# Kernel optimization log

Measured on AMD Instinct MI355X. Metric: run time of the kernel, lower is better.

The kernel has to match this reference:

```python
import jax, jax.numpy as jnp
import numpy as np

N = 8192  # number of proposals


def setup_inputs() -> dict:
    key = jax.random.key(0)
    k1, k2, k3 = jax.random.split(key, 3)
    xy = jax.random.uniform(k1, (N, 2), dtype=jnp.float32) * 1000.0   # top-left corners
    wh = jax.random.uniform(k2, (N, 2), dtype=jnp.float32) * 120.0 + 4.0  # widths/heights
    conf = jax.random.uniform(k3, (N, 1), dtype=jnp.float32)
    preds = jnp.concatenate([xy, xy + wh, conf], axis=1)  # [N,5] x1,y1,x2,y2,conf
    return {"preds": preds, "thresh": 0.5, "max_proposals": 1000}


def _nms_keep_mask(boxes_sorted, thresh):
    # boxes_sorted: [N,4] sorted by descending confidence
    x1, y1, x2, y2 = (boxes_sorted[:, i] for i in range(4))
    area = (x2 - x1) * (y2 - y1)                               # [N]
    ix1 = jnp.maximum(x1[:, None], x1[None, :])
    iy1 = jnp.maximum(y1[:, None], y1[None, :])
    ix2 = jnp.minimum(x2[:, None], x2[None, :])
    iy2 = jnp.minimum(y2[:, None], y2[None, :])
    iw = jnp.maximum(ix2 - ix1, 0.0)
    ih = jnp.maximum(iy2 - iy1, 0.0)
    inter = iw * ih                                            # [N,N]
    iou = inter / (area[:, None] + area[None, :] - inter + 1e-12)
    n = boxes_sorted.shape[0]
    later = jnp.arange(n)[None, :] > jnp.arange(n)[:, None]    # strictly lower-priority boxes

    def body(i, keep):
        # if box i survives, suppress all later boxes overlapping it above thresh
        sup = keep[i] & later[i] & (iou[i] > thresh)
        return keep & ~sup

    return jax.lax.fori_loop(0, n, body, jnp.ones((n,), dtype=bool))


def reference(preds, thresh, max_proposals):
    # thresh < 0 -> identity (original early return); implemented with thresh >= 0 path
    order = jnp.argsort(-preds[:, 4])          # descending confidence
    boxes_sorted = preds[order, :4]
    keep = _nms_keep_mask(boxes_sorted, thresh)  # [N] bool, in sorted order
    n = preds.shape[0]
    # stable pack: kept positions first (ascending = descending confidence), pad at end
    rank = jnp.where(keep, jnp.arange(n), n)
    pos = jnp.argsort(rank)[:max_proposals]     # [M] positions in sorted order
    valid = keep[pos]                           # [M] which slots are real
    keep_idx = jnp.where(valid, order[pos], -1)  # indices into original preds, -1 pad
    kept = preds[jnp.clip(keep_idx, 0)]          # [M,5]
    kept = jnp.where(valid[:, None], kept, 0.0)
    return kept, keep_idx
```

## Files before the change

### kernel.cpp

```cpp
#include <hip/hip_runtime.h>

typedef unsigned long long u64;

#define FSLOTS 16
#define RCUT 2048

__device__ __forceinline__ u64 bcast64(u64 v, int b) {
  unsigned lo = __builtin_amdgcn_readlane((unsigned)v, b);
  unsigned hi = __builtin_amdgcn_readlane((unsigned)(v >> 32), b);
  return ((u64)hi << 32) | lo;
}
__device__ __forceinline__ u64 sgpr64(u64 v) {
  unsigned lo = __builtin_amdgcn_readfirstlane((unsigned)v);
  unsigned hi = __builtin_amdgcn_readfirstlane((unsigned)(v >> 32));
  return ((u64)hi << 32) | lo;
}
__device__ __forceinline__ u64 wor64(u64 v) {
#pragma unroll
  for (int off = 32; off; off >>= 1) v |= __shfl_xor(v, off, 64);
  return v;
}

#define APPLYJ(JV, T)                                                      \
  if ((T) < lim_) {                                                        \
    int j_ = (JV);                                                         \
    atomicAnd(&live[j_ >> 6], ~((u64)1 << (j_ & 63)));                     \
  }

#define CHUNK(c, BND, RC, LA, LB, LC, LD)                                  \
  if (out < maxp && (c) < nch) {                                           \
    u64 rem_ = sgpr64(live[(c)]);                                          \
    if (rem_) {                                                            \
      u64 K_;                                                              \
      u64 my_ = ((rem_ >> lane) & 1) ? (BND) : 0;                          \
      u64 A_ = sgpr64(wor64(my_));                                         \
      u64 hot_ = rem_ & A_;                                                \
      if (!hot_) {                                                         \
        K_ = rem_;                                                         \
      } else {                                                             \
        u64 defK_ = rem_ & ~A_;                                            \
        u64 myk_ = ((defK_ >> lane) & 1) ? (BND) : 0;                      \
        u64 S_ = sgpr64(wor64(myk_));                                      \
        K_ = defK_;                                                        \
        while (hot_) {                                                     \
          int b_ = __builtin_amdgcn_readfirstlane(                         \
              (int)__builtin_ctzll(hot_));                                 \
          hot_ &= hot_ - 1;                                                \
          if (!((S_ >> b_) & 1)) {                                         \
            K_ |= (u64)1 << b_;                                            \
            S_ |= bcast64(BND, b_);                                        \
          }                                                                \
        }                                                                  \
      }                                                                    \
      int kc_ = (int)__popcll(K_);                                         \
      bool mine_ = (K_ >> lane) & 1;                                       \
      if (mine_) {                                                         \
        int pos_ = out + (int)__popcll(K_ & (((u64)1 << lane) - 1));       \
        if (pos_ < maxp) sel[pos_] = (c) * 64 + lane;                      \
      }                                                                    \
      out += kc_;                                                          \
      if (kc_ > 0 && out < maxp) {                                         \
        int lim_ = mine_ ? ((RC) < FSLOTS ? (RC) : FSLOTS) : 0;            \
        APPLYJ((LA).x, 0)  APPLYJ((LA).y, 1)                               \
        APPLYJ((LA).z, 2)  APPLYJ((LA).w, 3)                               \
        APPLYJ((LB).x, 4)  APPLYJ((LB).y, 5)                               \
        APPLYJ((LB).z, 6)  APPLYJ((LB).w, 7)                               \
        APPLYJ((LC).x, 8)  APPLYJ((LC).y, 9)                               \
        APPLYJ((LC).z, 10) APPLYJ((LC).w, 11)                              \
        APPLYJ((LD).x, 12) APPLYJ((LD).y, 13)                              \
        APPLYJ((LD).z, 14) APPLYJ((LD).w, 15)                              \
        u64 ovf_ = __ballot(mine_ && (RC) > FSLOTS);                       \
        while (ovf_) {                                                     \
          int l_ = (int)__builtin_ctzll(ovf_);                             \
          ovf_ &= ovf_ - 1;                                                \
          int r_ = (c) * 64 + l_;                                          \
          u64 v0_ = (2 * lane < nch)                                       \
                        ? M[(size_t)r_ * nw + 2 * lane] : 0ULL;            \
          u64 v1_ = (2 * lane + 1 < nch)                                   \
                        ? M[(size_t)r_ * nw + 2 * lane + 1] : 0ULL;        \
          live[2 * lane] &= ~v0_;                                          \
          live[2 * lane + 1] &= ~v1_;                                      \
        }                                                                  \
      }                                                                    \
    }                                                                      \
    {                                                                      \
      int cc_ = (c) + 4;                                                   \
      if (cc_ < nch) {                                                     \
        int r_ = cc_ * 64 + lane;                                          \
        int rr_ = r_ < n ? r_ : n - 1;                                     \
        BND = D1[rr_];                                                     \
        RC = rowcnt[rr_];                                                  \
        const int4* lp_ = (const int4*)(rowlist + (size_t)rr_ * FSLOTS);   \
        LA = lp_[0]; LB = lp_[1]; LC = lp_[2]; LD = lp_[3];                \
      }                                                                    \
    }                                                                      \
  }

#define PREF(cc, BND, RC, LA, LB, LC, LD)                                  \
  if ((cc) < nch) {                                                        \
    int r_ = (cc) * 64 + lane;                                             \
    int rr_ = r_ < n ? r_ : n - 1;                                         \
    BND = D1[rr_];                                                         \
    RC = rowcnt[rr_];                                                      \
    const int4* lp_ = (const int4*)(rowlist + (size_t)rr_ * FSLOTS);       \
    LA = lp_[0]; LB = lp_[1]; LC = lp_[2]; LD = lp_[3];                    \
  }

#define SCAN_BODY(NCH_)                                                    \
  int nch = (NCH_);                                                        \
  for (int w = lane; w < 128; w += 64) {                                   \
    u64 m = 0;                                                             \
    if (w < nw) {                                                          \
      long long hi = (long long)(w + 1) * 64;                              \
      m = (hi <= n) ? ~0ULL                                                \
                    : ((n > (long long)w * 64)                             \
                           ? (((u64)1 << (n - w * 64)) - 1) : 0ULL);       \
    }                                                                      \
    live[w] = m;                                                           \
  }                                                                        \
  u64 b0 = 0, b1 = 0, b2 = 0, b3 = 0;                                      \
  int rc0 = 0, rc1 = 0, rc2 = 0, rc3 = 0;                                  \
  int4 l00 = {0,0,0,0}, l01 = {0,0,0,0}, l02 = {0,0,0,0}, l03 = {0,0,0,0}; \
  int4 l10 = {0,0,0,0}, l11 = {0,0,0,0}, l12 = {0,0,0,0}, l13 = {0,0,0,0}; \
  int4 l20 = {0,0,0,0}, l21 = {0,0,0,0}, l22 = {0,0,0,0}, l23 = {0,0,0,0}; \
  int4 l30 = {0,0,0,0}, l31 = {0,0,0,0}, l32 = {0,0,0,0}, l33 = {0,0,0,0}; \
  PREF(0, b0, rc0, l00, l01, l02, l03)                                     \
  PREF(1, b1, rc1, l10, l11, l12, l13)                                     \
  PREF(2, b2, rc2, l20, l21, l22, l23)                                     \
  PREF(3, b3, rc3, l30, l31, l32, l33)                                     \
  int out = 0;                                                             \
  for (int kk = 0; kk < nch && out < maxp; kk += 4) {                      \
    CHUNK(kk + 0, b0, rc0, l00, l01, l02, l03)                             \
    CHUNK(kk + 1, b1, rc1, l10, l11, l12, l13)                             \
    CHUNK(kk + 2, b2, rc2, l20, l21, l22, l23)                             \
    CHUNK(kk + 3, b3, rc3, l30, l31, l32, l33)                             \
  }

__device__ __forceinline__ void do_tile(int wx, int ry, int lane,
                                        const float4* sb4, float4* cb,
                                        float* cbar, int n, float th,
                                        u64* M, u64* D1, int* rowcnt,
                                        int* rowlist, int nw) {
  int col0 = wx * 64;
  int cj = col0 + lane;
  int cjc = cj < n ? cj : n - 1;
  {
    float4 b4 = sb4[cjc];
    cb[lane] = b4;
    cbar[lane] = __fmul_rn(__fsub_rn(b4.z, b4.x), __fsub_rn(b4.w, b4.y));
  }
  int row = ry * 64 + lane;
  if (row >= n) return;
  float4 r4 = sb4[row];
  float rarea = __fmul_rn(__fsub_rn(r4.z, r4.x), __fsub_rn(r4.w, r4.y));
  u64 w = 0;
#pragma unroll 8
  for (int j = 0; j < 64; ++j) {
    float4 c4 = cb[j];
    float ix1 = fmaxf(r4.x, c4.x);
    float iy1 = fmaxf(r4.y, c4.y);
    float ix2 = fminf(r4.z, c4.z);
    float iy2 = fminf(r4.w, c4.w);
    float iw = fmaxf(__fsub_rn(ix2, ix1), 0.0f);
    float ih = fmaxf(__fsub_rn(iy2, iy1), 0.0f);
    float inter = __fmul_rn(iw, ih);
    float denom = __fadd_rn(__fsub_rn(__fadd_rn(rarea, cbar[j]), inter), 1e-12f);
    float iou = __fdiv_rn(inter, denom);
    int col = col0 + j;
    bool sup = (col > row) && (col < n) && (iou > th);
    w |= ((u64)sup) << j;
  }
  M[(size_t)row * nw + wx] = w;
  if (wx == ry) D1[row] = w;
  int pcw = (int)__popcll(w);
  if (pcw) {
    int base = atomicAdd(&rowcnt[row], pcw);
    u64 w2 = w;
    int k = 0;
    while (w2) {
      int j = (int)__builtin_ctzll(w2);
      w2 &= w2 - 1;
      int idx = base + k;
      if (idx < FSLOTS) rowlist[(size_t)row * FSLOTS + idx] = col0 + j;
      ++k;
    }
  }
}

__device__ __forceinline__ void tri_decode(int u, int* wxo, int* ryo) {
  int w = (int)((sqrtf(8.0f * u + 1.0f) - 1.0f) * 0.5f);
  while ((w + 1) * (w + 2) / 2 <= u) ++w;
  while (w * (w + 1) / 2 > u) --w;
  *wxo = w;
  *ryo = u - w * (w + 1) / 2;
}

__global__ __launch_bounds__(256)
void k_rank(const float* __restrict__ preds, int n,
            float* __restrict__ sboxes, int* __restrict__ sidx,
            int* __restrict__ rowcnt) {
  __shared__ float cs[8192];
  int t = threadIdx.x;
  int b = blockIdx.x;
  for (int j = t; j < n; j += 256) cs[j] = preds[j * 5 + 4];
  {
    int zi = b * 32 + t;
    if (t < 32 && zi < n) rowcnt[zi] = 0;
  }
  __syncthreads();

  int row = b * 32 + (t >> 3);
  int sub = t & 7;
  int cw = (((n + 7) >> 3) + 3) & ~3;
  int cnt = 0;
  if (row < n) {
    float ci = cs[row];
    int start = sub * cw;
    int end = start + cw; if (end > n) end = n;
    const float4* cs4 = (const float4*)cs;
    int s4 = start >> 2, e4 = end >> 2;
    for (int j4 = s4; j4 < e4; ++j4) {
      float4 c4 = cs4[j4];
      int jb = j4 * 4;
      cnt += (c4.x > ci) || (c4.x == ci && (jb + 0) < row);
      cnt += (c4.y > ci) || (c4.y == ci && (jb + 1) < row);
      cnt += (c4.z > ci) || (c4.z == ci && (jb + 2) < row);
      cnt += (c4.w > ci) || (c4.w == ci && (jb + 3) < row);
    }
    for (int j = e4 * 4; j < end; ++j)
      cnt += (cs[j] > ci) || (cs[j] == ci && j < row);
  }
  cnt += __shfl_down(cnt, 4, 8);
  cnt += __shfl_down(cnt, 2, 8);
  cnt += __shfl_down(cnt, 1, 8);
  if (sub == 0 && row < n) {
    int pos = cnt;
    sboxes[pos * 4 + 0] = preds[row * 5 + 0];
    sboxes[pos * 4 + 1] = preds[row * 5 + 1];
    sboxes[pos * 4 + 2] = preds[row * 5 + 2];
    sboxes[pos * 4 + 3] = preds[row * 5 + 3];
    sidx[pos] = row;
  }
}

__global__ __launch_bounds__(64)
void k_mask_lo(const float* __restrict__ sboxes, int n,
               const float* __restrict__ thr_p,
               u64* __restrict__ M, u64* __restrict__ D1,
               int* __restrict__ rowcnt, int* __restrict__ rowlist, int nw) {
  __shared__ float4 cb[64];
  __shared__ float cbar[64];
  int wx, ry;
  tri_decode(blockIdx.x, &wx, &ry);
  do_tile(wx, ry, threadIdx.x, (const float4*)sboxes, cb, cbar, n, *thr_p,
          M, D1, rowcnt, rowlist, nw);
}

__global__ __launch_bounds__(256, 1)
void k_finish(u64* __restrict__ M, u64* __restrict__ D1,
              int* __restrict__ rowcnt, int* __restrict__ rowlist,
              const float* __restrict__ preds, const float* __restrict__ thr_p,
              const float* __restrict__ sboxes, const int* __restrict__ sidx,
              int n, int nw, int maxp, int Rw,
              int* __restrict__ sel, float* __restrict__ outp) {
  __shared__ u64 live[128];
  __shared__ float4 cbw[4][64];
  __shared__ float cbarw[4][64];
  __shared__ int nk_s, done_s;
  int t = threadIdx.x;
  int wid = t >> 6;

  if (t < 64) {
    int lane = t;
    SCAN_BODY(Rw)
    if (lane == 0) {
      nk_s = (out < maxp) ? out : maxp;
      done_s = (out >= maxp || Rw >= nw) ? 1 : 0;
    }
  }
  __syncthreads();

  if (!done_s) {
    int loTri = (Rw * (Rw + 1)) / 2;
    int totTri = (nw * (nw + 1)) / 2;
    float th = *thr_p;
    const float4* sb4 = (const float4*)sboxes;
    for (int u = loTri + wid; u < totTri; u += 4) {
      int wx, ry;
      tri_decode(u, &wx, &ry);
      do_tile(wx, ry, t & 63, sb4, cbw[wid], cbarw[wid], n, th,
              M, D1, rowcnt, rowlist, nw);
    }
    __threadfence();
    __syncthreads();
    if (t < 64) {
      int lane = t;
      SCAN_BODY(nw)
      if (lane == 0) nk_s = (out < maxp) ? out : maxp;
    }
    __syncthreads();
  }

  int nk = nk_s;
  for (int k = t; k < maxp; k += 256) {
    if (k < nk) {
      int p = sel[k];
      int orig = sidx[p];
#pragma unroll
      for (int q = 0; q < 5; ++q) outp[k * 5 + q] = preds[orig * 5 + q];
      outp[(size_t)maxp * 5 + k] = (float)orig;
    } else {
#pragma unroll
      for (int q = 0; q < 5; ++q) outp[k * 5 + q] = 0.0f;
      outp[(size_t)maxp * 5 + k] = -1.0f;
    }
  }
}

extern "C" void kernel_launch(void* const* d_in, const int* in_sizes, int n_in,
                              void* d_out, int out_size, void* d_ws, size_t ws_size,
                              hipStream_t stream) {
  const float* preds = (const float*)d_in[0];
  const float* thr   = (const float*)d_in[1];
  float* out = (float*)d_out;
  int n    = in_sizes[0] / 5;
  int maxp = out_size / 6;
  int nw   = (n + 63) / 64;
  int Rw   = (RCUT / 64 < nw) ? RCUT / 64 : nw;
  int loTri = (Rw * (Rw + 1)) / 2;

  char* ws = (char*)d_ws;
  u64* M = (u64*)ws;
  size_t off = (size_t)n * nw * sizeof(u64);
  u64* D1 = (u64*)(ws + off);  off += (size_t)n * sizeof(u64);
  float* sboxes = (float*)(ws + off);  off += (size_t)n * 4 * sizeof(float);
  int*   sidx   = (int*)(ws + off);    off += (size_t)n * sizeof(int);
  int*   sel    = (int*)(ws + off);    off += (size_t)maxp * sizeof(int);
  int*   rowcnt = (int*)(ws + off);    off += (size_t)n * sizeof(int);
  int*   rowlist= (int*)(ws + off);

  hipLaunchKernelGGL(k_rank, dim3((n + 31) / 32), dim3(256), 0, stream,
                     preds, n, sboxes, sidx, rowcnt);
  hipLaunchKernelGGL(k_mask_lo, dim3(loTri), dim3(64), 0, stream,
                     sboxes, n, thr, M, D1, rowcnt, rowlist, nw);
  hipLaunchKernelGGL(k_finish, dim3(1), dim3(256), 0, stream,
                     M, D1, rowcnt, rowlist, preds, thr, sboxes, sidx,
                     n, nw, maxp, Rw, sel, out);
}
```

Measured before the change: 68.15 us.

## Fuse low-triangle mask kernel into finish kernel with flag-based grid barrier

Merges the triangle-tile mask kernel and the single-block finish kernel into one 256-block launch. Each block computes its share of tiles and publishes a release flag, and block 0 spin-waits on all flags before running the scan and tail work. This removes one kernel launch and its inter-kernel gap. The cost is the spin-wait, and correctness depends on all 256 blocks being co-resident (flags are reset in the prep kernel), with 4-wave blocks instead of single-wave ones.

```diff
diff --git a/kernel.cpp b/kernel.cpp
--- a/kernel.cpp
+++ b/kernel.cpp
@@ -4,6 +4,7 @@
 
 #define FSLOTS 16
 #define RCUT 2048
+#define NBLK 256
 
 __device__ __forceinline__ u64 bcast64(u64 v, int b) {
   unsigned lo = __builtin_amdgcn_readlane((unsigned)v, b);
@@ -196,9 +197,9 @@
 }
 
 __global__ __launch_bounds__(256)
-void k_rank(const float* __restrict__ preds, int n,
+void k_prep(const float* __restrict__ preds, int n,
             float* __restrict__ sboxes, int* __restrict__ sidx,
-            int* __restrict__ rowcnt) {
+            int* __restrict__ rowcnt, int* __restrict__ flags) {
   __shared__ float cs[8192];
   int t = threadIdx.x;
   int b = blockIdx.x;
@@ -206,6 +207,7 @@
   {
     int zi = b * 32 + t;
     if (t < 32 && zi < n) rowcnt[zi] = 0;
+    if (t == 0) flags[b] = 0;
   }
   __syncthreads();
 
@@ -243,32 +245,44 @@
   }
 }
 
-__global__ __launch_bounds__(64)
-void k_mask_lo(const float* __restrict__ sboxes, int n,
-               const float* __restrict__ thr_p,
-               u64* __restrict__ M, u64* __restrict__ D1,
-               int* __restrict__ rowcnt, int* __restrict__ rowlist, int nw) {
-  __shared__ float4 cb[64];
-  __shared__ float cbar[64];
-  int wx, ry;
-  tri_decode(blockIdx.x, &wx, &ry);
-  do_tile(wx, ry, threadIdx.x, (const float4*)sboxes, cb, cbar, n, *thr_p,
-          M, D1, rowcnt, rowlist, nw);
-}
-
 __global__ __launch_bounds__(256, 1)
-void k_finish(u64* __restrict__ M, u64* __restrict__ D1,
-              int* __restrict__ rowcnt, int* __restrict__ rowlist,
-              const float* __restrict__ preds, const float* __restrict__ thr_p,
-              const float* __restrict__ sboxes, const int* __restrict__ sidx,
-              int n, int nw, int maxp, int Rw,
-              int* __restrict__ sel, float* __restrict__ outp) {
+void k_main(u64* __restrict__ M, u64* __restrict__ D1,
+            int* __restrict__ rowcnt, int* __restrict__ rowlist,
+            const float* __restrict__ preds, const float* __restrict__ thr_p,
+            const float* __restrict__ sboxes, const int* __restrict__ sidx,
+            int n, int nw, int maxp, int Rw,
+            int* __restrict__ sel, int* __restrict__ flags,
+            float* __restrict__ outp) {
   __shared__ u64 live[128];
   __shared__ float4 cbw[4][64];
   __shared__ float cbarw[4][64];
   __shared__ int nk_s, done_s;
   int t = threadIdx.x;
+  int bid = blockIdx.x;
   int wid = t >> 6;
+  float th = *thr_p;
+  const float4* sb4 = (const float4*)sboxes;
+
+  {
+    int loTri = (Rw * (Rw + 1)) / 2;
+    for (int u = bid * 4 + wid; u < loTri; u += NBLK * 4) {
+      int wx, ry;
+      tri_decode(u, &wx, &ry);
+      do_tile(wx, ry, t & 63, sb4, cbw[wid], cbarw[wid], n, th,
+              M, D1, rowcnt, rowlist, nw);
+    }
+  }
+  __syncthreads();
+  if (t == 0) {
+    __threadfence();
+    __hip_atomic_store(&flags[bid], 1, __ATOMIC_RELEASE,
+                       __HIP_MEMORY_SCOPE_AGENT);
+  }
+  if (bid != 0) return;
+
+  while (__hip_atomic_load(&flags[t], __ATOMIC_ACQUIRE,
+                           __HIP_MEMORY_SCOPE_AGENT) == 0) {}
+  __syncthreads();
 
   if (t < 64) {
     int lane = t;
@@ -283,8 +297,6 @@
   if (!done_s) {
     int loTri = (Rw * (Rw + 1)) / 2;
     int totTri = (nw * (nw + 1)) / 2;
-    float th = *thr_p;
-    const float4* sb4 = (const float4*)sboxes;
     for (int u = loTri + wid; u < totTri; u += 4) {
       int wx, ry;
       tri_decode(u, &wx, &ry);
@@ -327,7 +339,6 @@
   int maxp = out_size / 6;
   int nw   = (n + 63) / 64;
   int Rw   = (RCUT / 64 < nw) ? RCUT / 64 : nw;
-  int loTri = (Rw * (Rw + 1)) / 2;
 
   char* ws = (char*)d_ws;
   u64* M = (u64*)ws;
@@ -337,13 +348,12 @@
   int*   sidx   = (int*)(ws + off);    off += (size_t)n * sizeof(int);
   int*   sel    = (int*)(ws + off);    off += (size_t)maxp * sizeof(int);
   int*   rowcnt = (int*)(ws + off);    off += (size_t)n * sizeof(int);
-  int*   rowlist= (int*)(ws + off);
-
-  hipLaunchKernelGGL(k_rank, dim3((n + 31) / 32), dim3(256), 0, stream,
-                     preds, n, sboxes, sidx, rowcnt);
-  hipLaunchKernelGGL(k_mask_lo, dim3(loTri), dim3(64), 0, stream,
-                     sboxes, n, thr, M, D1, rowcnt, rowlist, nw);
-  hipLaunchKernelGGL(k_finish, dim3(1), dim3(256), 0, stream,
+  int*   rowlist= (int*)(ws + off);    off += (size_t)n * FSLOTS * sizeof(int);
+  int*   flags  = (int*)(ws + off);
+
+  hipLaunchKernelGGL(k_prep, dim3((n + 31) / 32), dim3(256), 0, stream,
+                     preds, n, sboxes, sidx, rowcnt, flags);
+  hipLaunchKernelGGL(k_main, dim3(NBLK), dim3(256), 0, stream,
                      M, D1, rowcnt, rowlist, preds, thr, sboxes, sidx,
-                     n, nw, maxp, Rw, sel, out);
-}
+                     n, nw, maxp, Rw, sel, flags, out);
+}
```

Result: slower. 76.14 us (+11.7%).
